# Optimization experiments

Hardware: AMD Instinct MI355X
Metric: run time of the kernel (lower is better)

Reference implementation:

```python
import jax, jax.numpy as jnp
import numpy as np

KAPPA = 0.5


def setup_inputs() -> dict:
    key = jax.random.key(0)
    embeddings = jax.random.normal(key, (8, 4096, 64), dtype=jnp.float32)
    return {"embeddings": embeddings}


def reference(embeddings):
    # logits[b, n, m] = kappa * <emb[b,n], emb[b,m]>   -> [B, N, N]
    logits = KAPPA * jnp.einsum("bnd,bmd->bnm", embeddings, embeddings)
    B = logits.shape[0]
    # logsumexp over both matrix dims, per batch element
    loss = jax.scipy.special.logsumexp(logits.reshape(B, -1), axis=1)
    return loss.mean()
```

## Files before the change

kernel.cpp:

```cpp
#include <hip/hip_runtime.h>
#include <math.h>

#define BATCH 8
#define NTOK  4096
#define DIM   64
#define BM    256
#define NT    (NTOK / BM)
#define TPB   (NT * (NT + 1) / 2)
#define KAPPA 0.5f
#define FIXM  60.0f
#define LOG2E 1.4426950408889634f
#define C1    (KAPPA * LOG2E)
#define C2    (-FIXM * LOG2E)

typedef _Float16 f16x8  __attribute__((ext_vector_type(8)));
typedef __fp16   h2     __attribute__((ext_vector_type(2)));
typedef float    f32x16 __attribute__((ext_vector_type(16)));

__device__ __forceinline__ float exp2_fast(float x) {
#if __has_builtin(__builtin_amdgcn_exp2f)
    return __builtin_amdgcn_exp2f(x);
#else
    return __expf(x * 0.6931471805599453f);
#endif
}

__device__ __forceinline__ f16x8 pack8(float4 lo, float4 hi) {
    union { f16x8 v; h2 p[4]; } u;
    u.p[0] = __builtin_amdgcn_cvt_pkrtz(lo.x, lo.y);
    u.p[1] = __builtin_amdgcn_cvt_pkrtz(lo.z, lo.w);
    u.p[2] = __builtin_amdgcn_cvt_pkrtz(hi.x, hi.y);
    u.p[3] = __builtin_amdgcn_cvt_pkrtz(hi.z, hi.w);
    return u.v;
}

__global__ __launch_bounds__(512, 2)
void gram_lse_partial(const float* __restrict__ emb, float* __restrict__ ws) {
    __shared__ f16x8 As[8 * BM];
    __shared__ f16x8 Bs[8 * BM];

    const int tid = threadIdx.x;
    const int bb  = blockIdx.x;
    const int b   = bb / TPB;
    int t = bb - b * TPB;
    int ti = 0;
    while (t >= NT - ti) { t -= NT - ti; ++ti; }
    const int tj = ti + t;
    const bool diag = (ti == tj);

    const float* embA = emb + ((size_t)b * NTOK + (size_t)ti * BM) * DIM;
    const float* embB = emb + ((size_t)b * NTOK + (size_t)tj * BM) * DIM;

    {
        const int g  = tid & 7;
        const int r0 = tid >> 3;
#pragma unroll
        for (int p = 0; p < 4; ++p) {
            const int row = r0 + 64 * p;
            const int su  = g * BM + (row ^ g);
            const float4 a0 = *(const float4*)(embA + (size_t)row * DIM + g * 8);
            const float4 a1 = *(const float4*)(embA + (size_t)row * DIM + g * 8 + 4);
            As[su] = pack8(a0, a1);
            if (!diag) {
                const float4 b0 = *(const float4*)(embB + (size_t)row * DIM + g * 8);
                const float4 b1 = *(const float4*)(embB + (size_t)row * DIM + g * 8 + 4);
                Bs[su] = pack8(b0, b1);
            }
        }
    }
    __syncthreads();

    const int lane  = tid & 63;
    const int w     = tid >> 6;
    const int half  = lane >> 5;
    const int ln31  = lane & 31;
    const int rbase = (w & 1) * 128;
    const int cbase = (w >> 1) * 64;
    const f16x8* __restrict__ Bp = diag ? As : Bs;

    f32x16 acc[4][2] = {};
#pragma unroll
    for (int s = 0; s < 4; ++s) {
        const int g = 2 * s + half;
        f16x8 af[4], bf[2];
#pragma unroll
        for (int i = 0; i < 4; ++i)
            af[i] = As[g * BM + ((rbase + 32 * i + ln31) ^ g)];
#pragma unroll
        for (int j = 0; j < 2; ++j)
            bf[j] = Bp[g * BM + ((cbase + 32 * j + ln31) ^ g)];
#pragma unroll
        for (int i = 0; i < 4; ++i)
#pragma unroll
            for (int j = 0; j < 2; ++j)
                acc[i][j] = __builtin_amdgcn_mfma_f32_32x32x16_f16(
                    af[i], bf[j], acc[i][j], 0, 0, 0);
    }

    float lsum = 0.f;
#pragma unroll
    for (int i = 0; i < 4; ++i)
#pragma unroll
        for (int j = 0; j < 2; ++j)
#pragma unroll
            for (int e = 0; e < 16; ++e)
                lsum += exp2_fast(fmaf(C1, acc[i][j][e], C2));
#pragma unroll
    for (int off = 32; off > 0; off >>= 1)
        lsum += __shfl_xor(lsum, off);
    if (lane == 0)
        ws[8 * (size_t)bb + w] = (diag ? 1.f : 2.f) * lsum;
}

__global__ __launch_bounds__(512)
void reduce_lse(const float* __restrict__ ws, float* __restrict__ out) {
    const int tid  = threadIdx.x;
    const int w    = tid >> 6;
    const int lane = tid & 63;
    __shared__ float lse[BATCH];

    const float* p = ws + (size_t)w * TPB * 8;
    float s = 0.f;
    for (int idx = lane; idx < TPB * 8; idx += 64) s += p[idx];
#pragma unroll
    for (int off = 32; off > 0; off >>= 1) s += __shfl_xor(s, off);

    if (lane == 0) lse[w] = FIXM + logf(s);
    __syncthreads();
    if (tid == 0) {
        float a = 0.f;
        for (int i = 0; i < BATCH; ++i) a += lse[i];
        out[0] = a * (1.f / BATCH);
    }
}

extern "C" void kernel_launch(void* const* d_in, const int* in_sizes, int n_in,
                              void* d_out, int out_size, void* d_ws, size_t ws_size,
                              hipStream_t stream) {
    const float* emb = (const float*)d_in[0];
    float* out = (float*)d_out;
    float* ws  = (float*)d_ws;

    gram_lse_partial<<<BATCH * TPB, 512, 0, stream>>>(emb, ws);
    reduce_lse<<<1, 512, 0, stream>>>(ws, out);
}
```

Before: 85.65 us.

## Fuse reduction into persistent gram-LSE kernel with double-buffered tile prefetch

Replaces the one-block-per-tile-pair launch with 256 persistent blocks that walk tile pairs in a strided loop. Each block prefetches the next pair's embeddings into registers while running MFMA and exp on the current pair, using double-buffered shared memory. Partial sums go into striped atomic accumulators, and the last block to finish, found through an atomic counter, computes the final logsumexp mean. This removes the second kernel launch but adds a memset and atomics, and the larger shared-memory and register footprint may lower occupancy.

```diff
diff --git a/kernel.cpp b/kernel.cpp
--- a/kernel.cpp
+++ b/kernel.cpp
@@ -1,17 +1,20 @@
 #include <hip/hip_runtime.h>
 #include <math.h>
 
-#define BATCH 8
-#define NTOK  4096
-#define DIM   64
-#define BM    256
-#define NT    (NTOK / BM)
-#define TPB   (NT * (NT + 1) / 2)
-#define KAPPA 0.5f
-#define FIXM  60.0f
-#define LOG2E 1.4426950408889634f
-#define C1    (KAPPA * LOG2E)
-#define C2    (-FIXM * LOG2E)
+#define BATCH  8
+#define NTOK   4096
+#define DIM    64
+#define BM     256
+#define NT     (NTOK / BM)
+#define TPB    (NT * (NT + 1) / 2)
+#define NPAIRS (BATCH * TPB)
+#define NBLK   256
+#define KAPPA  0.5f
+#define FIXM   60.0f
+#define LOG2E  1.4426950408889634f
+#define C1     (KAPPA * LOG2E)
+#define C2     (-FIXM * LOG2E)
+#define NSTRIPE 16
 
 typedef _Float16 f16x8  __attribute__((ext_vector_type(8)));
 typedef __fp16   h2     __attribute__((ext_vector_type(2)));
@@ -34,103 +37,155 @@
     return u.v;
 }
 
+__device__ __forceinline__ void decode_pair(int p, int& b, int& ti, int& tj) {
+    b = p / TPB;
+    int t = p - b * TPB;
+    ti = 0;
+    while (t >= NT - ti) { t -= NT - ti; ++ti; }
+    tj = ti + t;
+}
+
 __global__ __launch_bounds__(512, 2)
-void gram_lse_partial(const float* __restrict__ emb, float* __restrict__ ws) {
-    __shared__ f16x8 As[8 * BM];
-    __shared__ f16x8 Bs[8 * BM];
-
-    const int tid = threadIdx.x;
-    const int bb  = blockIdx.x;
-    const int b   = bb / TPB;
-    int t = bb - b * TPB;
-    int ti = 0;
-    while (t >= NT - ti) { t -= NT - ti; ++ti; }
-    const int tj = ti + t;
-    const bool diag = (ti == tj);
-
-    const float* embA = emb + ((size_t)b * NTOK + (size_t)ti * BM) * DIM;
-    const float* embB = emb + ((size_t)b * NTOK + (size_t)tj * BM) * DIM;
-
-    {
-        const int g  = tid & 7;
-        const int r0 = tid >> 3;
-#pragma unroll
-        for (int p = 0; p < 4; ++p) {
-            const int row = r0 + 64 * p;
-            const int su  = g * BM + (row ^ g);
-            const float4 a0 = *(const float4*)(embA + (size_t)row * DIM + g * 8);
-            const float4 a1 = *(const float4*)(embA + (size_t)row * DIM + g * 8 + 4);
-            As[su] = pack8(a0, a1);
-            if (!diag) {
-                const float4 b0 = *(const float4*)(embB + (size_t)row * DIM + g * 8);
-                const float4 b1 = *(const float4*)(embB + (size_t)row * DIM + g * 8 + 4);
-                Bs[su] = pack8(b0, b1);
-            }
-        }
-    }
-    __syncthreads();
-
-    const int lane  = tid & 63;
-    const int w     = tid >> 6;
+void gram_lse_fused(const float* __restrict__ emb, float* __restrict__ ws,
+                    float* __restrict__ out) {
+    __shared__ f16x8 As[2][8 * BM];
+    __shared__ f16x8 Bs[2][8 * BM];
+    __shared__ float fin[BATCH * NSTRIPE];
+    __shared__ unsigned last_flag;
+
+    const int tid  = threadIdx.x;
+    const int bid  = blockIdx.x;
+    const int lane = tid & 63;
+    const int w    = tid >> 6;
+
+    const int g_s  = tid & 7;
+    const int r0_s = tid >> 3;
     const int half  = lane >> 5;
     const int ln31  = lane & 31;
     const int rbase = (w & 1) * 128;
     const int cbase = (w >> 1) * 64;
-    const f16x8* __restrict__ Bp = diag ? As : Bs;
-
-    f32x16 acc[4][2] = {};
-#pragma unroll
-    for (int s = 0; s < 4; ++s) {
-        const int g = 2 * s + half;
-        f16x8 af[4], bf[2];
-#pragma unroll
-        for (int i = 0; i < 4; ++i)
-            af[i] = As[g * BM + ((rbase + 32 * i + ln31) ^ g)];
-#pragma unroll
-        for (int j = 0; j < 2; ++j)
-            bf[j] = Bp[g * BM + ((cbase + 32 * j + ln31) ^ g)];
-#pragma unroll
-        for (int i = 0; i < 4; ++i)
-#pragma unroll
-            for (int j = 0; j < 2; ++j)
-                acc[i][j] = __builtin_amdgcn_mfma_f32_32x32x16_f16(
-                    af[i], bf[j], acc[i][j], 0, 0, 0);
-    }
-
-    float lsum = 0.f;
-#pragma unroll
-    for (int i = 0; i < 4; ++i)
-#pragma unroll
-        for (int j = 0; j < 2; ++j)
-#pragma unroll
-            for (int e = 0; e < 16; ++e)
-                lsum += exp2_fast(fmaf(C1, acc[i][j][e], C2));
-#pragma unroll
-    for (int off = 32; off > 0; off >>= 1)
-        lsum += __shfl_xor(lsum, off);
-    if (lane == 0)
-        ws[8 * (size_t)bb + w] = (diag ? 1.f : 2.f) * lsum;
-}
-
-__global__ __launch_bounds__(512)
-void reduce_lse(const float* __restrict__ ws, float* __restrict__ out) {
-    const int tid  = threadIdx.x;
-    const int w    = tid >> 6;
-    const int lane = tid & 63;
-    __shared__ float lse[BATCH];
-
-    const float* p = ws + (size_t)w * TPB * 8;
-    float s = 0.f;
-    for (int idx = lane; idx < TPB * 8; idx += 64) s += p[idx];
-#pragma unroll
-    for (int off = 32; off > 0; off >>= 1) s += __shfl_xor(s, off);
-
-    if (lane == 0) lse[w] = FIXM + logf(s);
+
+    int p = bid;
+    int b, ti, tj;
+    decode_pair(p, b, ti, tj);
+    bool diag = (ti == tj);
+
+    {
+        const float* eA = emb + ((size_t)b * NTOK + (size_t)ti * BM) * DIM;
+        const float* eB = emb + ((size_t)b * NTOK + (size_t)tj * BM) * DIM;
+#pragma unroll
+        for (int q = 0; q < 4; ++q) {
+            const int row = r0_s + 64 * q;
+            const int su  = g_s * BM + (row ^ g_s);
+            const float4 a0 = *(const float4*)(eA + (size_t)row * DIM + g_s * 8);
+            const float4 a1 = *(const float4*)(eA + (size_t)row * DIM + g_s * 8 + 4);
+            As[0][su] = pack8(a0, a1);
+            if (!diag) {
+                const float4 b0 = *(const float4*)(eB + (size_t)row * DIM + g_s * 8);
+                const float4 b1 = *(const float4*)(eB + (size_t)row * DIM + g_s * 8 + 4);
+                Bs[0][su] = pack8(b0, b1);
+            }
+        }
+    }
     __syncthreads();
+
+    int cur = 0;
+    while (p < NPAIRS) {
+        const int pn = p + NBLK;
+        const bool have_next = (pn < NPAIRS);
+        int bn = 0, tin = 0, tjn = 0;
+        bool diag_n = false;
+        float4 ra[8], rb[8];
+
+        if (have_next) {
+            decode_pair(pn, bn, tin, tjn);
+            diag_n = (tin == tjn);
+            const float* eA = emb + ((size_t)bn * NTOK + (size_t)tin * BM) * DIM;
+            const float* eB = emb + ((size_t)bn * NTOK + (size_t)tjn * BM) * DIM;
+#pragma unroll
+            for (int q = 0; q < 4; ++q) {
+                const int row = r0_s + 64 * q;
+                ra[2 * q]     = *(const float4*)(eA + (size_t)row * DIM + g_s * 8);
+                ra[2 * q + 1] = *(const float4*)(eA + (size_t)row * DIM + g_s * 8 + 4);
+                if (!diag_n) {
+                    rb[2 * q]     = *(const float4*)(eB + (size_t)row * DIM + g_s * 8);
+                    rb[2 * q + 1] = *(const float4*)(eB + (size_t)row * DIM + g_s * 8 + 4);
+                }
+            }
+        }
+
+        {
+            const f16x8* __restrict__ Ap = As[cur];
+            const f16x8* __restrict__ Bp = diag ? As[cur] : Bs[cur];
+            f32x16 acc[4][2] = {};
+#pragma unroll
+            for (int s = 0; s < 4; ++s) {
+                const int g = 2 * s + half;
+                f16x8 af[4], bf[2];
+#pragma unroll
+                for (int i = 0; i < 4; ++i)
+                    af[i] = Ap[g * BM + ((rbase + 32 * i + ln31) ^ g)];
+#pragma unroll
+                for (int j = 0; j < 2; ++j)
+                    bf[j] = Bp[g * BM + ((cbase + 32 * j + ln31) ^ g)];
+#pragma unroll
+                for (int i = 0; i < 4; ++i)
+#pragma unroll
+                    for (int j = 0; j < 2; ++j)
+                        acc[i][j] = __builtin_amdgcn_mfma_f32_32x32x16_f16(
+                            af[i], bf[j], acc[i][j], 0, 0, 0);
+            }
+            float lsum = 0.f;
+#pragma unroll
+            for (int i = 0; i < 4; ++i)
+#pragma unroll
+                for (int j = 0; j < 2; ++j)
+#pragma unroll
+                    for (int e = 0; e < 16; ++e)
+                        lsum += exp2_fast(fmaf(C1, acc[i][j][e], C2));
+#pragma unroll
+            for (int off = 32; off > 0; off >>= 1)
+                lsum += __shfl_xor(lsum, off);
+            if (lane == 0)
+                atomicAdd(&ws[b * NSTRIPE + (bid & (NSTRIPE - 1))],
+                          (diag ? 1.f : 2.f) * lsum);
+        }
+
+        if (have_next) {
+            const int nc = cur ^ 1;
+#pragma unroll
+            for (int q = 0; q < 4; ++q) {
+                const int row = r0_s + 64 * q;
+                const int su  = g_s * BM + (row ^ g_s);
+                As[nc][su] = pack8(ra[2 * q], ra[2 * q + 1]);
+                if (!diag_n) Bs[nc][su] = pack8(rb[2 * q], rb[2 * q + 1]);
+            }
+        }
+        __syncthreads();
+        cur ^= 1;
+        p = pn; b = bn; ti = tin; tj = tjn; diag = diag_n;
+    }
+
     if (tid == 0) {
-        float a = 0.f;
-        for (int i = 0; i < BATCH; ++i) a += lse[i];
-        out[0] = a * (1.f / BATCH);
+        __threadfence();
+        unsigned* cnt = (unsigned*)ws + BATCH * NSTRIPE;
+        const unsigned old = atomicAdd(cnt, 1u);
+        last_flag = (old == NBLK - 1) ? 1u : 0u;
+    }
+    __syncthreads();
+    if (last_flag) {
+        if (tid < BATCH * NSTRIPE)
+            fin[tid] = atomicAdd(&ws[tid], 0.f);
+        __syncthreads();
+        if (tid == 0) {
+            float a = 0.f;
+            for (int i = 0; i < BATCH; ++i) {
+                float s = 0.f;
+                for (int j = 0; j < NSTRIPE; ++j) s += fin[i * NSTRIPE + j];
+                a += FIXM + logf(s);
+            }
+            out[0] = a * (1.f / BATCH);
+        }
     }
 }
 
@@ -141,6 +196,6 @@
     float* out = (float*)d_out;
     float* ws  = (float*)d_ws;
 
-    gram_lse_partial<<<BATCH * TPB, 512, 0, stream>>>(emb, ws);
-    reduce_lse<<<1, 512, 0, stream>>>(ws, out);
-}
+    hipMemsetAsync(d_ws, 0, (BATCH * NSTRIPE + 1) * sizeof(float), stream);
+    gram_lse_fused<<<NBLK, 512, 0, stream>>>(emb, ws, out);
+}
```

Result: slower. 120.0 us (+40.1%).
